# Optimization experiments

Hardware: AMD Instinct MI355X
Metric: run time of the kernel (lower is better)

The kernel has to match this reference:

```python
import jax, jax.numpy as jnp
import numpy as np

N = 100000   # nodes
E = 3200000  # edges (before self-loops)
IN, H, OUT = 128, 256, 40

def glorot(key, shape):
    lim = (6.0 / (shape[0] + shape[1])) ** 0.5
    return jax.random.uniform(key, shape, jnp.float32, -lim, lim)

def setup_inputs() -> dict:
    key = jax.random.key(0)
    ks = jax.random.split(key, 8)
    x = jax.random.normal(ks[0], (N, IN), jnp.float32)
    edge_index = jax.random.randint(ks[1], (2, E), 0, N, dtype=jnp.int32)
    return {
        "x": x,
        "edge_index": edge_index,
        "W0": glorot(ks[2], (IN, H)),  "b0": jnp.zeros((H,), jnp.float32),
        "W1": glorot(ks[3], (H, H)),   "b1": jnp.zeros((H,), jnp.float32),
        "W2": glorot(ks[4], (H, OUT)), "b2": jnp.zeros((OUT,), jnp.float32),
    }

def _gcn_norm(edge_index, n):
    # PyG gcn_norm: add self-loops, symmetric D^{-1/2} A D^{-1/2}
    loops = jnp.arange(n, dtype=edge_index.dtype)
    src = jnp.concatenate([edge_index[0], loops])
    dst = jnp.concatenate([edge_index[1], loops])
    deg = jax.ops.segment_sum(jnp.ones_like(src, jnp.float32), dst, num_segments=n)
    dinv = jnp.where(deg > 0, jax.lax.rsqrt(deg), 0.0)
    norm = dinv[src] * dinv[dst]  # [E+N]
    return src, dst, norm

def _gcn_layer(h, W, b, src, dst, norm, n):
    h = h @ W                                   # transform first (PyG order)
    msg = h[src] * norm[:, None]                # gather + scale
    agg = jax.ops.segment_sum(msg, dst, num_segments=n)  # scatter-add
    return agg + b

def reference(x, edge_index, W0, b0, W1, b1, W2, b2):
    n = x.shape[0]
    src, dst, norm = _gcn_norm(edge_index, n)
    h = jnp.tanh(_gcn_layer(x, W0, b0, src, dst, norm, n))  # dropout = identity (eval)
    h = jnp.tanh(_gcn_layer(h, W1, b1, src, dst, norm, n))
    out = _gcn_layer(h, W2, b2, src, dst, norm, n)
    return jax.nn.log_softmax(out, axis=1)
```

## Files before the change

kernel.cpp:

```cpp
#include <hip/hip_runtime.h>
#include <hip/hip_bf16.h>
#include <cmath>


typedef unsigned short u16;
typedef __attribute__((ext_vector_type(8))) short short8;
typedef __attribute__((ext_vector_type(4))) float f32x4;

#define BSHIFT 10
#define BNODES (1 << BSHIFT)
#define ECAP   36864
#define BMASK 0x00FF00FFu

__device__ __forceinline__ u16 f2bf(float f) {
    unsigned int u = __float_as_uint(f);
    u += 0x7fffu + ((u >> 16) & 1u);
    return (u16)(u >> 16);
}

__device__ __forceinline__ int q8(float v) {
    return (int)rintf(fminf(fmaxf(v, -127.0f), 127.0f));
}


__global__ __launch_bounds__(128) void init_gcur_kernel(
        int* __restrict__ gcur, int nb) {
    int b = blockIdx.x * 128 + threadIdx.x;
    if (b < nb) gcur[b] = b * ECAP;
}

__global__ __launch_bounds__(256) void bucketize_kernel(
        const int* __restrict__ src, const int* __restrict__ dst,
        int* __restrict__ gcur, unsigned int* __restrict__ ebuf, int E) {
    __shared__ int cnt[128];
    __shared__ int base[128];
    int tid = threadIdx.x;
    int chunk0 = blockIdx.x * 8192;
    int cend = min(chunk0 + 8192, E);
    for (int r0 = chunk0; r0 < cend; r0 += 2048) {
        if (tid < 128) cnt[tid] = 0;
        __syncthreads();
        int rank[8], bk[8];
        unsigned int pk[8];
#pragma unroll
        for (int j = 0; j < 8; j++) {
            int e = r0 + j * 256 + tid;
            bk[j] = -1;
            if (e < cend) {
                int d = dst[e];
                bk[j] = d >> BSHIFT;
                pk[j] = (unsigned int)src[e] | ((unsigned int)(d & (BNODES - 1)) << 17);
                rank[j] = atomicAdd(&cnt[bk[j]], 1);
            }
        }
        __syncthreads();
        if (tid < 128 && cnt[tid] > 0) base[tid] = atomicAdd(&gcur[tid], cnt[tid]);
        __syncthreads();
#pragma unroll
        for (int j = 0; j < 8; j++)
            if (bk[j] >= 0) ebuf[base[bk[j]] + rank[j]] = pk[j];
        __syncthreads();
    }
}

__global__ __launch_bounds__(256) void deg_hist_kernel(
        const unsigned int* __restrict__ ebuf, const int* __restrict__ gcur,
        int* __restrict__ degi, float* __restrict__ dinv, int N) {
    __shared__ int h[BNODES];
    int b = blockIdx.x;
    int nb0 = b << BSHIFT;
    int nodes = min(BNODES, N - nb0);
    for (int i = threadIdx.x; i < nodes; i += 256) h[i] = 0;
    __syncthreads();
    int estart = b * ECAP;
    int eend = gcur[b];
    for (int e = estart + threadIdx.x; e < eend; e += 256)
        atomicAdd(&h[ebuf[e] >> 17], 1);
    __syncthreads();
    for (int i = threadIdx.x; i < nodes; i += 256) {
        int d = h[i];
        degi[nb0 + i] = d;
        dinv[nb0 + i] = rsqrtf((float)d + 1.0f);
    }
}

__global__ __launch_bounds__(256) void scan_part_kernel(
        const int* __restrict__ deg, int* __restrict__ part, int n) {
    __shared__ int s[256];
    int i = blockIdx.x * 256 + threadIdx.x;
    s[threadIdx.x] = (i < n) ? deg[i] : 0;
    __syncthreads();
    for (int off = 128; off; off >>= 1) {
        if (threadIdx.x < off) s[threadIdx.x] += s[threadIdx.x + off];
        __syncthreads();
    }
    if (threadIdx.x == 0) part[blockIdx.x] = s[0];
}

__global__ __launch_bounds__(256) void scan_apply_kernel(
        const int* __restrict__ deg, const int* __restrict__ part,
        int* __restrict__ rs, int n) {
    __shared__ int s[256];
    __shared__ int ps[256];
    int pp = 0;
    for (int j = threadIdx.x; j < blockIdx.x; j += 256) pp += part[j];
    ps[threadIdx.x] = pp;
    __syncthreads();
    for (int off = 128; off; off >>= 1) {
        if (threadIdx.x < off) ps[threadIdx.x] += ps[threadIdx.x + off];
        __syncthreads();
    }
    int base = ps[0];
    int i = blockIdx.x * 256 + threadIdx.x;
    int v = (i < n) ? deg[i] : 0;
    s[threadIdx.x] = v;
    __syncthreads();
    for (int off = 1; off < 256; off <<= 1) {
        int u = (threadIdx.x >= off) ? s[threadIdx.x - off] : 0;
        __syncthreads();
        s[threadIdx.x] += u;
        __syncthreads();
    }
    if (i < n) rs[i] = base + s[threadIdx.x] - v;
}

__global__ __launch_bounds__(256) void csr_fill_kernel(
        const unsigned int* __restrict__ ebuf, const int* __restrict__ gcur,
        const int* __restrict__ rs, int* __restrict__ csr, int N) {
    __shared__ int lcur[BNODES];
    int b = blockIdx.x;
    int nb0 = b << BSHIFT;
    int nodes = min(BNODES, N - nb0);
    for (int i = threadIdx.x; i < nodes; i += 256) lcur[i] = rs[nb0 + i];
    __syncthreads();
    int estart = b * ECAP;
    int eend = gcur[b];
    for (int e = estart + threadIdx.x; e < eend; e += 256) {
        unsigned int v = ebuf[e];
        int s = v & 0x1FFFF;
        int dl = v >> 17;
        int pos = atomicAdd(&lcur[dl], 1);
        csr[pos] = s;
    }
}

__global__ __launch_bounds__(256) void wt_all_kernel(
        const float* __restrict__ W0, const float* __restrict__ W1,
        const float* __restrict__ W2, u16* __restrict__ Wt0,
        u16* __restrict__ Wt1, u16* __restrict__ Wt2) {
    int i = blockIdx.x * 256 + threadIdx.x;
    if (i < 32768) {
        int k = i >> 8, c = i & 255;
        Wt0[c * 128 + k] = f2bf(W0[i]);
    } else if (i < 98304) {
        int j = i - 32768;
        int k = j >> 8, c = j & 255;
        Wt1[c * 256 + k] = f2bf(W1[j]);
    } else if (i < 108544) {
        int j = i - 98304;
        int k = j / 40, c = j - k * 40;
        Wt2[c * 256 + k] = f2bf(W2[j]);
    }
}

__global__ __launch_bounds__(256) void scale_x_kernel(
        const float* __restrict__ x, const float* __restrict__ dinv,
        unsigned int* __restrict__ out, int total4) {
    int i = blockIdx.x * 256 + threadIdx.x;
    if (i >= total4) return;
    int n = i >> 5;
    float4 v = reinterpret_cast<const float4*>(x)[i];
    float s = dinv[n] * 63.5f;
    int a0 = q8(v.x * s), a1 = q8(v.y * s), a2 = q8(v.z * s), a3 = q8(v.w * s);
    out[i] = (unsigned int)(a0 & 0xff) | ((unsigned int)(a1 & 0xff) << 8) |
             ((unsigned int)(a2 & 0xff) << 16) | ((unsigned int)(a3 & 0xff) << 24);
}

#define ACC8(q0, q1)                                                  \
    do {                                                              \
        aex += (q0) & BMASK; aox += ((q0) >> 8) & BMASK;              \
        aey += (q1) & BMASK; aoy += ((q1) >> 8) & BMASK;              \
    } while (0)

__global__ __launch_bounds__(256) void agg128_i8_kernel(
        const signed char* __restrict__ in, u16* __restrict__ out,
        const int* __restrict__ rs, const int* __restrict__ deg,
        const int* __restrict__ csr, const float* __restrict__ dinv, int n) {
    int wid = blockIdx.x * 4 + (threadIdx.x >> 6);
    if (wid >= n) return;
    int lane = threadIdx.x & 63;
    int quad = lane >> 4;
    int l16 = lane & 15;
    int start = rs[wid];
    int cnt = deg[wid];

    unsigned int aex = 0, aox = 0, aey = 0, aoy = 0;
    if (quad == 0) {
        uint2 q = *reinterpret_cast<const uint2*>(
            in + (size_t)wid * 128 + l16 * 8);
        q.x ^= 0x80808080u; q.y ^= 0x80808080u;
        ACC8(q.x, q.y);
    }
    int i = 0;
    for (; i + 16 <= cnt; i += 16) {
        int s[4];
#pragma unroll
        for (int j = 0; j < 4; j++) s[j] = csr[start + i + 4 * j + quad];
#pragma unroll
        for (int j = 0; j < 4; j++) {
            uint2 q = *reinterpret_cast<const uint2*>(
                in + (size_t)s[j] * 128 + l16 * 8);
            q.x ^= 0x80808080u; q.y ^= 0x80808080u;
            ACC8(q.x, q.y);
        }
    }
    for (; i + 4 <= cnt; i += 4) {
        int s0 = csr[start + i + quad];
        uint2 q = *reinterpret_cast<const uint2*>(
            in + (size_t)s0 * 128 + l16 * 8);
        q.x ^= 0x80808080u; q.y ^= 0x80808080u;
        ACC8(q.x, q.y);
    }
    int rem = cnt - i;
    if (quad < rem) {
        int s0 = csr[start + i + quad];
        uint2 q = *reinterpret_cast<const uint2*>(
            in + (size_t)s0 * 128 + l16 * 8);
        q.x ^= 0x80808080u; q.y ^= 0x80808080u;
        ACC8(q.x, q.y);
    }
    aex += (unsigned int)__shfl((int)aex, lane + 32);
    aox += (unsigned int)__shfl((int)aox, lane + 32);
    aey += (unsigned int)__shfl((int)aey, lane + 32);
    aoy += (unsigned int)__shfl((int)aoy, lane + 32);
    aex += (unsigned int)__shfl((int)aex, lane + 16);
    aox += (unsigned int)__shfl((int)aox, lane + 16);
    aey += (unsigned int)__shfl((int)aey, lane + 16);
    aoy += (unsigned int)__shfl((int)aoy, lane + 16);
    if (lane < 16) {
        int T = cnt + 1;
        int bias = 128 * T;
        float c = dinv[wid] * (2.0f / 127.0f);
        float f0 = (float)((int)(aex & 0xFFFFu) - bias) * c;
        float f1 = (float)((int)(aox & 0xFFFFu) - bias) * c;
        float f2 = (float)((int)(aex >> 16) - bias) * c;
        float f3 = (float)((int)(aox >> 16) - bias) * c;
        float f4 = (float)((int)(aey & 0xFFFFu) - bias) * c;
        float f5 = (float)((int)(aoy & 0xFFFFu) - bias) * c;
        float f6 = (float)((int)(aey >> 16) - bias) * c;
        float f7 = (float)((int)(aoy >> 16) - bias) * c;
        uint4 o;
        o.x = (unsigned)f2bf(f0) | ((unsigned)f2bf(f1) << 16);
        o.y = (unsigned)f2bf(f2) | ((unsigned)f2bf(f3) << 16);
        o.z = (unsigned)f2bf(f4) | ((unsigned)f2bf(f5) << 16);
        o.w = (unsigned)f2bf(f6) | ((unsigned)f2bf(f7) << 16);
        reinterpret_cast<uint4*>(out + (size_t)wid * 128)[l16] = o;
    }
}

__global__ __launch_bounds__(256) void agg_i8_kernel(
        const signed char* __restrict__ in, u16* __restrict__ out,
        const int* __restrict__ rs, const int* __restrict__ deg,
        const int* __restrict__ csr, const float* __restrict__ dinv, int n) {
    int wid = blockIdx.x * 4 + (threadIdx.x >> 6);
    if (wid >= n) return;
    int lane = threadIdx.x & 63;
    int start = rs[wid];
    int cnt = deg[wid];

    unsigned int q = *reinterpret_cast<const unsigned int*>(
        in + (size_t)wid * 256 + lane * 4) ^ 0x80808080u;
    unsigned int ae = q & BMASK, ao = (q >> 8) & BMASK;

    int i = 0;
    for (; i + 16 <= cnt; i += 16) {
        int s[16];
#pragma unroll
        for (int j = 0; j < 16; j++)
            s[j] = __builtin_amdgcn_readfirstlane(csr[start + i + j]);
        unsigned int qq[16];
#pragma unroll
        for (int j = 0; j < 16; j++)
            qq[j] = *reinterpret_cast<const unsigned int*>(
                in + (size_t)s[j] * 256 + lane * 4);
#pragma unroll
        for (int j = 0; j < 16; j++) {
            unsigned int v = qq[j] ^ 0x80808080u;
            ae += v & BMASK;
            ao += (v >> 8) & BMASK;
        }
    }
    if (i < cnt) {
        int s[16];
#pragma unroll
        for (int j = 0; j < 16; j++) {
            int e = i + j;
            e = (e < cnt) ? e : (cnt - 1);
            s[j] = __builtin_amdgcn_readfirstlane(csr[start + e]);
        }
        unsigned int qq[16];
#pragma unroll
        for (int j = 0; j < 16; j++)
            qq[j] = *reinterpret_cast<const unsigned int*>(
                in + (size_t)s[j] * 256 + lane * 4);
#pragma unroll
        for (int j = 0; j < 16; j++) {
            unsigned int m = (i + j < cnt) ? 0xFFFFFFFFu : 0u;
            unsigned int v = (qq[j] ^ 0x80808080u) & m;
            ae += v & BMASK;
            ao += (v >> 8) & BMASK;
        }
    }

    int bias = 128 * (cnt + 1);
    float c = dinv[wid] * (1.0f / 127.0f);
    float f0 = (float)((int)(ae & 0xFFFFu) - bias) * c;
    float f1 = (float)((int)(ao & 0xFFFFu) - bias) * c;
    float f2 = (float)((int)(ae >> 16) - bias) * c;
    float f3 = (float)((int)(ao >> 16) - bias) * c;
    uint2 o;
    o.x = (unsigned)f2bf(f0) | ((unsigned)f2bf(f1) << 16);
    o.y = (unsigned)f2bf(f2) | ((unsigned)f2bf(f3) << 16);
    reinterpret_cast<uint2*>(out + (size_t)wid * 256)[lane] = o;
}

template<int EPI, typename CT>
__global__ __launch_bounds__(256) void mfma_mm_kernel(
        const u16* __restrict__ A, const u16* __restrict__ Bt,
        CT* __restrict__ C, int M, int K, int NC,
        const float* __restrict__ bias, const float* __restrict__ postscale,
        float qs) {
    __shared__ u16 As[128 * 40];
    __shared__ u16 Bs[64 * 40];
    int t = threadIdx.x;
    int w = t >> 6, lane = t & 63, quad = lane >> 4, l16 = lane & 15;
    int row0 = blockIdx.x * 128;
    int col0 = blockIdx.y * 64;

    f32x4 acc[2][4];
#pragma unroll
    for (int s = 0; s < 2; s++)
#pragma unroll
        for (int nb = 0; nb < 4; nb++)
            acc[s][nb] = (f32x4){0.f, 0.f, 0.f, 0.f};

    int bn = t >> 2, bkq = (t & 3) << 3;
    for (int k0 = 0; k0 < K; k0 += 32) {
#pragma unroll
        for (int i = t; i < 512; i += 256) {
            int r = i >> 2, c = (i & 3) << 3;
            int gr = row0 + r;
            uint4 v = {0u, 0u, 0u, 0u};
            if (gr < M)
                v = *reinterpret_cast<const uint4*>(A + (size_t)gr * K + k0 + c);
            *reinterpret_cast<uint4*>(&As[r * 40 + c]) = v;
        }
        {
            int gc = col0 + bn;
            uint4 v = {0u, 0u, 0u, 0u};
            if (gc < NC)
                v = *reinterpret_cast<const uint4*>(Bt + (size_t)gc * K + k0 + bkq);
            *reinterpret_cast<uint4*>(&Bs[bn * 40 + bkq]) = v;
        }
        __syncthreads();

        short8 af[2], bf[4];
        af[0] = *reinterpret_cast<const short8*>(&As[(w * 32 + l16) * 40 + quad * 8]);
        af[1] = *reinterpret_cast<const short8*>(&As[(w * 32 + 16 + l16) * 40 + quad * 8]);
#pragma unroll
        for (int nb = 0; nb < 4; nb++)
            bf[nb] = *reinterpret_cast<const short8*>(&Bs[(nb * 16 + l16) * 40 + quad * 8]);
#pragma unroll
        for (int s = 0; s < 2; s++)
#pragma unroll
            for (int nb = 0; nb < 4; nb++)
                acc[s][nb] = __builtin_amdgcn_mfma_f32_16x16x32_bf16(
                    af[s], bf[nb], acc[s][nb], 0, 0, 0);
        __syncthreads();
    }

#pragma unroll
    for (int s = 0; s < 2; s++) {
        int rbase = row0 + w * 32 + s * 16 + quad * 4;
#pragma unroll
        for (int nb = 0; nb < 4; nb++) {
            int gc = col0 + nb * 16 + l16;
#pragma unroll
            for (int r = 0; r < 4; r++) {
                int gr = rbase + r;
                if (gr >= M || gc >= NC) continue;
                float v = acc[s][nb][r];
                if constexpr (EPI == 1) v = tanhf(v + bias[gc]);
                else                    v = v * postscale[gr];
                if constexpr (sizeof(CT) == 1) {
                    float m = qs;
                    if constexpr (EPI == 1) m *= postscale[gr];
                    C[(size_t)gr * NC + gc] = (CT)q8(v * m);
                } else {
                    C[(size_t)gr * NC + gc] = (CT)f2bf(v);
                }
            }
        }
    }
}

__global__ __launch_bounds__(256) void agg40_ls_kernel(
        const signed char* __restrict__ in, const int* __restrict__ rs,
        const int* __restrict__ deg, const int* __restrict__ csr,
        const float* __restrict__ dinv, const float* __restrict__ bias,
        float* __restrict__ out, int n) {
    int wid = blockIdx.x * 4 + (threadIdx.x >> 6);
    if (wid >= n) return;
    int lane = threadIdx.x & 63;
    int grp = lane / 5;
    int l5 = lane - grp * 5;
    bool act = lane < 60;
    int start = rs[wid];
    int cnt = deg[wid];

    unsigned int aex = 0, aox = 0, aey = 0, aoy = 0;
    if (lane < 5) {
        uint2 q = *reinterpret_cast<const uint2*>(
            in + (size_t)wid * 40 + l5 * 8);
        q.x ^= 0x80808080u; q.y ^= 0x80808080u;
        ACC8(q.x, q.y);
    }
    for (int base = 0; base < cnt; base += 12) {
        int e = base + grp;
        if (act && e < cnt) {
            int s0 = csr[start + e];
            uint2 q = *reinterpret_cast<const uint2*>(
                in + (size_t)s0 * 40 + l5 * 8);
            q.x ^= 0x80808080u; q.y ^= 0x80808080u;
            ACC8(q.x, q.y);
        }
    }
    aex += (unsigned int)__shfl((int)aex, lane + 30);
    aox += (unsigned int)__shfl((int)aox, lane + 30);
    aey += (unsigned int)__shfl((int)aey, lane + 30);
    aoy += (unsigned int)__shfl((int)aoy, lane + 30);
    aex += (unsigned int)__shfl((int)aex, lane + 15);
    aox += (unsigned int)__shfl((int)aox, lane + 15);
    aey += (unsigned int)__shfl((int)aey, lane + 15);
    aoy += (unsigned int)__shfl((int)aoy, lane + 15);
    aex += (unsigned int)__shfl((int)aex, lane + 5) + (unsigned int)__shfl((int)aex, lane + 10);
    aox += (unsigned int)__shfl((int)aox, lane + 5) + (unsigned int)__shfl((int)aox, lane + 10);
    aey += (unsigned int)__shfl((int)aey, lane + 5) + (unsigned int)__shfl((int)aey, lane + 10);
    aoy += (unsigned int)__shfl((int)aoy, lane + 5) + (unsigned int)__shfl((int)aoy, lane + 10);

    bool act5 = lane < 5;
    float s = dinv[wid];
    float v0 = -INFINITY, v1 = -INFINITY, v2 = -INFINITY, v3 = -INFINITY;
    float v4 = -INFINITY, v5 = -INFINITY, v6 = -INFINITY, v7 = -INFINITY;
    if (act5) {
        int bb = 128 * (cnt + 1);
        float c = s * (1.0f / 63.0f);
        int cc = lane * 8;
        v0 = (float)((int)(aex & 0xFFFFu) - bb) * c + bias[cc + 0];
        v1 = (float)((int)(aox & 0xFFFFu) - bb) * c + bias[cc + 1];
        v2 = (float)((int)(aex >> 16) - bb) * c + bias[cc + 2];
        v3 = (float)((int)(aox >> 16) - bb) * c + bias[cc + 3];
        v4 = (float)((int)(aey & 0xFFFFu) - bb) * c + bias[cc + 4];
        v5 = (float)((int)(aoy & 0xFFFFu) - bb) * c + bias[cc + 5];
        v6 = (float)((int)(aey >> 16) - bb) * c + bias[cc + 6];
        v7 = (float)((int)(aoy >> 16) - bb) * c + bias[cc + 7];
    }
    float m = fmaxf(fmaxf(fmaxf(v0, v1), fmaxf(v2, v3)),
                    fmaxf(fmaxf(v4, v5), fmaxf(v6, v7)));
    for (int off = 4; off; off >>= 1) m = fmaxf(m, __shfl_xor(m, off));
    float e = 0.f;
    if (act5) e = __expf(v0 - m) + __expf(v1 - m) + __expf(v2 - m) + __expf(v3 - m)
                + __expf(v4 - m) + __expf(v5 - m) + __expf(v6 - m) + __expf(v7 - m);
    for (int off = 4; off; off >>= 1) e += __shfl_xor(e, off);
    float ls = logf(e);
    if (act5) {
        float4 o0, o1;
        o0.x = v0 - m - ls; o0.y = v1 - m - ls; o0.z = v2 - m - ls; o0.w = v3 - m - ls;
        o1.x = v4 - m - ls; o1.y = v5 - m - ls; o1.z = v6 - m - ls; o1.w = v7 - m - ls;
        float4* op = reinterpret_cast<float4*>(out + (size_t)wid * 40 + lane * 8);
        op[0] = o0;
        op[1] = o1;
    }
}

extern "C" void kernel_launch(void* const* d_in, const int* in_sizes, int n_in,
                              void* d_out, int out_size, void* d_ws, size_t ws_size,
                              hipStream_t stream) {
    const float* x  = (const float*)d_in[0];
    const int*   ei = (const int*)d_in[1];
    const float* W0 = (const float*)d_in[2];
    const float* b0 = (const float*)d_in[3];
    const float* W1 = (const float*)d_in[4];
    const float* b1 = (const float*)d_in[5];
    const float* W2 = (const float*)d_in[6];
    const float* b2 = (const float*)d_in[7];
    float* out = (float*)d_out;

    const int N = in_sizes[0] / 128;
    const int E = in_sizes[1] / 2;
    const int IN = 128, H = 256, OUT = 40;
    const int NB = (N + BNODES - 1) >> BSHIFT;

    char* p = (char*)d_ws;
    auto carve = [&](size_t bytes) -> void* {
        void* r = (void*)p;
        p += (bytes + 255) & ~(size_t)255;
        return r;
    };
    float*        dinv = (float*)carve((size_t)N * 4);
    int*          degi = (int*)  carve((size_t)N * 4);
    int*          rs   = (int*)  carve((size_t)N * 4);
    int*          part = (int*)  carve((size_t)1024 * 4);
    int*          gcur = (int*)  carve((size_t)128 * 4);
    int*          csr  = (int*)  carve((size_t)E * 4);
    unsigned int* ebuf = (unsigned int*)carve((size_t)NB * ECAP * 4);
    u16*          Wt0  = (u16*)  carve((size_t)IN * H * 2);
    u16*          Wt1  = (u16*)  carve((size_t)H * H * 2);
    u16*          Wt2  = (u16*)  carve((size_t)H * OUT * 2);
    u16*          U1   = (u16*)  carve((size_t)N * H * 2);
    u16*          U2   = (u16*)  carve((size_t)N * H * 2);

    signed char* Xq   = (signed char*)U1;
    u16*         T0bf = U1 + (size_t)N * IN / 2 + 64;
    signed char* H0q  = (signed char*)U2;
    u16*         T1bf = U1;
    u16*         h1bf = U2;
    signed char* G2q  = (signed char*)U1;

    const int* src = ei;
    const int* dst = ei + E;

    int gN = (N + 255) / 256;
    int gW = (N + 3) / 4;
    int gMM = (N + 127) / 128;
    int gA = (E + 8191) / 8192;

    init_gcur_kernel<<<1, 128, 0, stream>>>(gcur, NB);
    bucketize_kernel<<<gA, 256, 0, stream>>>(src, dst, gcur, ebuf, E);
    deg_hist_kernel<<<NB, 256, 0, stream>>>(ebuf, gcur, degi, dinv, N);
    scan_part_kernel<<<gN, 256, 0, stream>>>(degi, part, N);
    scan_apply_kernel<<<gN, 256, 0, stream>>>(degi, part, rs, N);
    csr_fill_kernel<<<NB, 256, 0, stream>>>(ebuf, gcur, rs, csr, N);

    wt_all_kernel<<<(108544 + 255) / 256, 256, 0, stream>>>(
        W0, W1, W2, Wt0, Wt1, Wt2);

    int t4x = N * (IN / 4);
    scale_x_kernel<<<(t4x + 255) / 256, 256, 0, stream>>>(
        x, dinv, (unsigned int*)Xq, t4x);
    agg128_i8_kernel<<<gW, 256, 0, stream>>>(Xq, T0bf, rs, degi, csr, dinv, N);
    mfma_mm_kernel<1, signed char><<<dim3(gMM, H / 64), 256, 0, stream>>>(
        T0bf, Wt0, H0q, N, IN, H, b0, dinv, 127.0f);

    agg_i8_kernel<<<gW, 256, 0, stream>>>(H0q, T1bf, rs, degi, csr, dinv, N);
    mfma_mm_kernel<1, u16><<<dim3(gMM, H / 64), 256, 0, stream>>>(
        T1bf, Wt1, h1bf, N, H, H, b1, nullptr, 0.f);

    mfma_mm_kernel<0, signed char><<<dim3(gMM, 1), 256, 0, stream>>>(
        h1bf, Wt2, G2q, N, H, OUT, nullptr, dinv, 63.0f);
    agg40_ls_kernel<<<gW, 256, 0, stream>>>(G2q, rs, degi, csr, dinv, b2, out, N);
}
```

Before: 614.5 us.

## Fuse degree histogram, prefix scan and CSR fill into one per-bucket kernel

Replaces the four CSR-building kernels (degree histogram, two-pass scan, CSR fill) with one kernel per 1024-node bucket. Each block derives its global edge offset from the bucket counters in gcur, scans its local histogram in shared memory, and fills the CSR directly. This removes three launches, the degi/rs round trips through global memory and the second read of ebuf. In exchange every block redundantly sums the preceding bucket counts, and only 98 blocks run the whole phase.

```diff
diff --git a/kernel.cpp b/kernel.cpp
--- a/kernel.cpp
+++ b/kernel.cpp
@@ -63,83 +63,69 @@
     }
 }
 
-__global__ __launch_bounds__(256) void deg_hist_kernel(
+__global__ __launch_bounds__(256) void bucket_csr_kernel(
         const unsigned int* __restrict__ ebuf, const int* __restrict__ gcur,
-        int* __restrict__ degi, float* __restrict__ dinv, int N) {
+        int* __restrict__ degi, float* __restrict__ dinv,
+        int* __restrict__ rs, int* __restrict__ csr, int N) {
     __shared__ int h[BNODES];
+    __shared__ int lp[BNODES];
+    __shared__ int ps[256];
     int b = blockIdx.x;
+    int t = threadIdx.x;
     int nb0 = b << BSHIFT;
     int nodes = min(BNODES, N - nb0);
-    for (int i = threadIdx.x; i < nodes; i += 256) h[i] = 0;
+
+    int acc = 0;
+    for (int j = t; j < b; j += 256) acc += gcur[j] - j * ECAP;
+    ps[t] = acc;
+    __syncthreads();
+    for (int off = 128; off; off >>= 1) {
+        if (t < off) ps[t] += ps[t + off];
+        __syncthreads();
+    }
+    int bbase = ps[0];
+    __syncthreads();
+
+    for (int i = t; i < BNODES; i += 256) h[i] = 0;
     __syncthreads();
     int estart = b * ECAP;
     int eend = gcur[b];
-    for (int e = estart + threadIdx.x; e < eend; e += 256)
+    for (int e = estart + t; e < eend; e += 256)
         atomicAdd(&h[ebuf[e] >> 17], 1);
     __syncthreads();
-    for (int i = threadIdx.x; i < nodes; i += 256) {
+
+    int a0 = h[t * 4], a1 = h[t * 4 + 1], a2 = h[t * 4 + 2], a3 = h[t * 4 + 3];
+    int tsum = a0 + a1 + a2 + a3;
+    ps[t] = tsum;
+    __syncthreads();
+    for (int off = 1; off < 256; off <<= 1) {
+        int u = (t >= off) ? ps[t - off] : 0;
+        __syncthreads();
+        ps[t] += u;
+        __syncthreads();
+    }
+    int texcl = ps[t] - tsum;
+    lp[t * 4]     = texcl;
+    lp[t * 4 + 1] = texcl + a0;
+    lp[t * 4 + 2] = texcl + a0 + a1;
+    lp[t * 4 + 3] = texcl + a0 + a1 + a2;
+    __syncthreads();
+
+    for (int i = t; i < nodes; i += 256) {
         int d = h[i];
         degi[nb0 + i] = d;
         dinv[nb0 + i] = rsqrtf((float)d + 1.0f);
-    }
-}
-
-__global__ __launch_bounds__(256) void scan_part_kernel(
-        const int* __restrict__ deg, int* __restrict__ part, int n) {
-    __shared__ int s[256];
-    int i = blockIdx.x * 256 + threadIdx.x;
-    s[threadIdx.x] = (i < n) ? deg[i] : 0;
-    __syncthreads();
-    for (int off = 128; off; off >>= 1) {
-        if (threadIdx.x < off) s[threadIdx.x] += s[threadIdx.x + off];
-        __syncthreads();
-    }
-    if (threadIdx.x == 0) part[blockIdx.x] = s[0];
-}
-
-__global__ __launch_bounds__(256) void scan_apply_kernel(
-        const int* __restrict__ deg, const int* __restrict__ part,
-        int* __restrict__ rs, int n) {
-    __shared__ int s[256];
-    __shared__ int ps[256];
-    int pp = 0;
-    for (int j = threadIdx.x; j < blockIdx.x; j += 256) pp += part[j];
-    ps[threadIdx.x] = pp;
-    __syncthreads();
-    for (int off = 128; off; off >>= 1) {
-        if (threadIdx.x < off) ps[threadIdx.x] += ps[threadIdx.x + off];
-        __syncthreads();
-    }
-    int base = ps[0];
-    int i = blockIdx.x * 256 + threadIdx.x;
-    int v = (i < n) ? deg[i] : 0;
-    s[threadIdx.x] = v;
-    __syncthreads();
-    for (int off = 1; off < 256; off <<= 1) {
-        int u = (threadIdx.x >= off) ? s[threadIdx.x - off] : 0;
-        __syncthreads();
-        s[threadIdx.x] += u;
-        __syncthreads();
-    }
-    if (i < n) rs[i] = base + s[threadIdx.x] - v;
-}
-
-__global__ __launch_bounds__(256) void csr_fill_kernel(
-        const unsigned int* __restrict__ ebuf, const int* __restrict__ gcur,
-        const int* __restrict__ rs, int* __restrict__ csr, int N) {
-    __shared__ int lcur[BNODES];
-    int b = blockIdx.x;
-    int nb0 = b << BSHIFT;
-    int nodes = min(BNODES, N - nb0);
-    for (int i = threadIdx.x; i < nodes; i += 256) lcur[i] = rs[nb0 + i];
-    __syncthreads();
-    int estart = b * ECAP;
-    int eend = gcur[b];
-    for (int e = estart + threadIdx.x; e < eend; e += 256) {
+        rs[nb0 + i] = bbase + lp[i];
+    }
+    __syncthreads();
+    for (int i = t; i < BNODES; i += 256) h[i] = bbase + lp[i];
+    __syncthreads();
+
+    for (int e = estart + t; e < eend; e += 256) {
         unsigned int v = ebuf[e];
         int s = v & 0x1FFFF;
         int dl = v >> 17;
-        int pos = atomicAdd(&lcur[dl], 1);
+        int pos = atomicAdd(&h[dl], 1);
         csr[pos] = s;
     }
 }
@@ -510,7 +496,6 @@
     float*        dinv = (float*)carve((size_t)N * 4);
     int*          degi = (int*)  carve((size_t)N * 4);
     int*          rs   = (int*)  carve((size_t)N * 4);
-    int*          part = (int*)  carve((size_t)1024 * 4);
     int*          gcur = (int*)  carve((size_t)128 * 4);
     int*          csr  = (int*)  carve((size_t)E * 4);
     unsigned int* ebuf = (unsigned int*)carve((size_t)NB * ECAP * 4);
@@ -530,17 +515,14 @@
     const int* src = ei;
     const int* dst = ei + E;
 
-    int gN = (N + 255) / 256;
     int gW = (N + 3) / 4;
     int gMM = (N + 127) / 128;
     int gA = (E + 8191) / 8192;
 
     init_gcur_kernel<<<1, 128, 0, stream>>>(gcur, NB);
     bucketize_kernel<<<gA, 256, 0, stream>>>(src, dst, gcur, ebuf, E);
-    deg_hist_kernel<<<NB, 256, 0, stream>>>(ebuf, gcur, degi, dinv, N);
-    scan_part_kernel<<<gN, 256, 0, stream>>>(degi, part, N);
-    scan_apply_kernel<<<gN, 256, 0, stream>>>(degi, part, rs, N);
-    csr_fill_kernel<<<NB, 256, 0, stream>>>(ebuf, gcur, rs, csr, N);
+    bucket_csr_kernel<<<NB, 256, 0, stream>>>(
+        ebuf, gcur, degi, dinv, rs, csr, N);
 
     wt_all_kernel<<<(108544 + 255) / 256, 256, 0, stream>>>(
         W0, W1, W2, Wt0, Wt1, Wt2);
```

Measured after the change: 605.5 us. No clear change (-1.5%).
